# Kernel tuning notes

Measured on AMD Instinct MI355X. Metric: run time of the kernel, lower is better.

Reference implementation:

```python
import jax, jax.numpy as jnp
import numpy as np

GAMMA = 0.01
INFER_STEP = 5


def softor(x, axis, gamma=GAMMA):
    # gamma * logsumexp(x / gamma) along `axis`, rescaled by global max if it exceeds 1
    y = gamma * jax.nn.logsumexp(x / gamma, axis=axis)
    mx = jnp.max(y)
    return jnp.where(mx > 1.0, y / mx, y)


def setup_inputs() -> dict:
    key = jax.random.key(0)
    k1, k2, k3 = jax.random.split(key, 3)
    B, G, C, S, L, m = 32, 2048, 16, 8, 3, 16
    x = jax.random.uniform(k1, (B, G), dtype=jnp.float32)          # valuation vector in [0,1]
    W = jax.random.normal(k2, (m, C), dtype=jnp.float32)           # clause-assignment weights
    I = jax.random.randint(k3, (C, G, S, L), 0, G)                 # index tensor into atom axis
    return {"x": x, "W": W, "I": I}


def reference(x, W, I):
    # x: [B,G] valuations; W: [m,C]; I: [C,G,S,L] int indices into G
    def r(V):
        # all C clause functions at once: gather V along atom axis using I
        gathered = V[:, I]                      # [B,C,G,S,L]
        body = jnp.prod(gathered, axis=-1)      # conjunction over body literals -> [B,C,G,S]
        Cv = softor(body, axis=-1)              # softor over substitutions -> [B,C,G]
        Ws = jax.nn.softmax(W, axis=1)          # [m,C]
        H = jnp.einsum('mc,bcg->mbg', Ws, Cv)   # weighted clause mix -> [m,B,G]
        return softor(H, axis=0)                # softor over m heads -> [B,G]

    R = x
    for _ in range(INFER_STEP):
        R = softor(jnp.stack([R, r(R)], axis=1), axis=1)  # amalgamate old and new facts
    return R
```

## Files before the change

kernel.cpp:

```cpp
#include <hip/hip_runtime.h>

#define GAMMA 0.01f
#define B 32
#define G 2048
#define C 16
#define S 8
#define L 3
#define M 16
#define NBLK 256
#define NTHR 256
#define SLOT_STRIDE 16

#define K_EXP 144.26950408889634f
#define K_LOG 0.006931471805599453f

#define SCOPE __HIP_MEMORY_SCOPE_AGENT

__device__ __forceinline__ void ast(unsigned* p, unsigned v) {
    __hip_atomic_store(p, v, __ATOMIC_RELAXED, SCOPE);
}
__device__ __forceinline__ float aldf(const float* p) {
    return __hip_atomic_load(p, __ATOMIC_RELAXED, SCOPE);
}
__device__ __forceinline__ void astf(float* p, float v) {
    __hip_atomic_store(p, v, __ATOMIC_RELAXED, SCOPE);
}

__device__ __forceinline__ float waveMax(float v) {
#pragma unroll
    for (int off = 32; off > 0; off >>= 1)
        v = fmaxf(v, __shfl_xor(v, off, 64));
    return v;
}

__device__ __forceinline__ float blockMaxBcast(float v, float* scratch) {
    float wm = waveMax(v);
    __syncthreads();
    if ((threadIdx.x & 63) == 0) scratch[threadIdx.x >> 6] = wm;
    __syncthreads();
    return fmaxf(fmaxf(scratch[0], scratch[1]), fmaxf(scratch[2], scratch[3]));
}

__device__ __forceinline__ float gridMaxBarrier(unsigned long long* slot,
                                                unsigned ep, float v,
                                                float* scratch) {
    float wm = waveMax(v);
    __syncthreads();
    if ((threadIdx.x & 63) == 0) scratch[threadIdx.x >> 6] = wm;
    __syncthreads();
    if (threadIdx.x == 0) {
        float bm = fmaxf(fmaxf(scratch[0], scratch[1]),
                         fmaxf(scratch[2], scratch[3]));
        unsigned long long pkt = ((unsigned long long)ep << 32) |
                                 (unsigned long long)__float_as_uint(bm);
        asm volatile("s_waitcnt vmcnt(0) lgkmcnt(0)" ::: "memory");
        __hip_atomic_store(&slot[(size_t)blockIdx.x * SLOT_STRIDE], pkt,
                           __ATOMIC_RELAXED, SCOPE);
    }
    unsigned long long got;
    int guard = 0;
    do {
        got = __hip_atomic_load(&slot[(size_t)threadIdx.x * SLOT_STRIDE],
                                __ATOMIC_RELAXED, SCOPE);
    } while ((unsigned)(got >> 32) < ep && ++guard < (1 << 17));
    return blockMaxBcast(__uint_as_float((unsigned)got), scratch);
}

extern "C" __global__ __launch_bounds__(256) void kmain(
    const float* __restrict__ x, const float* __restrict__ W,
    const int* __restrict__ I,
    unsigned long long* __restrict__ slotA, unsigned long long* __restrict__ slotB,
    unsigned long long* __restrict__ slotC, unsigned* __restrict__ Ipk,
    float* __restrict__ Ry, float* __restrict__ out)
{
    __shared__ __align__(16) float Vrow[G];
    __shared__ float WsL[C * M];
    __shared__ float scratch[4];

    const int t = threadIdx.x;
    const int bid = blockIdx.x;
    const int b = bid & 31;
    const int gt = bid >> 5;
    const int g = (gt << 8) + t;
    const int i = b * G + g;

    {
        const int m = t >> 4, c = t & 15;
        float rmax = -INFINITY;
#pragma unroll
        for (int j = 0; j < C; j++) rmax = fmaxf(rmax, W[m * C + j]);
        float rsum = 0.f;
#pragma unroll
        for (int j = 0; j < C; j++) rsum += __expf(W[m * C + j] - rmax);
        WsL[c * M + m] = __expf(W[m * C + c] - rmax) / rsum;
    }
    {
        const int tid = bid * NTHR + t;
        if (tid < C * G) {
            const int4* ip4 = (const int4*)(I + (size_t)tid * 24);
            int idx[24];
#pragma unroll
            for (int j = 0; j < 6; j++) {
                int4 v = ip4[j];
                idx[4 * j + 0] = v.x; idx[4 * j + 1] = v.y;
                idx[4 * j + 2] = v.z; idx[4 * j + 3] = v.w;
            }
            unsigned* dst = Ipk + (size_t)tid * 12;
#pragma unroll
            for (int j = 0; j < 12; j++)
                ast(&dst[j],
                    ((unsigned)idx[2 * j] << 2) | ((unsigned)idx[2 * j + 1] << 18));
        }
    }
    float m3 = gridMaxBarrier(slotC, 1, -INFINITY, scratch);

    float ry = 0.f;
    for (int it = 0; it < 5; it++) {
        float s = 1.0f;
        if (it > 0)
            s = (m3 > 1.0f) ? 1.0f / m3 : 1.0f;
        if (it == 0) {
            const float4* V4 = (const float4*)(x + (size_t)b * G);
            float4* Vr4 = (float4*)Vrow;
#pragma unroll
            for (int j = 0; j < 2; j++) Vr4[t + j * 256] = V4[t + j * 256];
        } else {
            const float* src = Ry + (size_t)b * G;
#pragma unroll
            for (int j = 0; j < 8; j++) {
                const int gg = t + j * 256;
                Vrow[gg] = s * aldf(&src[gg]);
            }
        }
        __syncthreads();

        float h[M];
#pragma unroll
        for (int m = 0; m < M; m++) h[m] = 0.f;
        float ymax = -INFINITY;
        const char* vb = (const char*)Vrow;

#pragma unroll 4
        for (int c = 0; c < C; c++) {
            const uint4* ip = (const uint4*)(Ipk + ((size_t)c * G + g) * 12);
            uint4 u0 = ip[0], u1 = ip[1], u2 = ip[2];
            unsigned w[12] = {u0.x, u0.y, u0.z, u0.w, u1.x, u1.y,
                              u1.z, u1.w, u2.x, u2.y, u2.z, u2.w};
            float vv[24];
#pragma unroll
            for (int q = 0; q < 12; q++) {
                vv[2 * q]     = *(const float*)(vb + (w[q] & 0xffffu));
                vv[2 * q + 1] = *(const float*)(vb + (w[q] >> 16));
            }
            float body[S];
#pragma unroll
            for (int ss = 0; ss < S; ss++)
                body[ss] = vv[ss * 3] * vv[ss * 3 + 1] * vv[ss * 3 + 2];
            float bm = body[0];
#pragma unroll
            for (int ss = 1; ss < S; ss++) bm = fmaxf(bm, body[ss]);
            float sum = 0.f;
#pragma unroll
            for (int ss = 0; ss < S; ss++)
                sum += exp2f((body[ss] - bm) * K_EXP);
            float y = fmaf(K_LOG, log2f(sum), bm);
            ymax = fmaxf(ymax, y);
#pragma unroll
            for (int m = 0; m < M; m++)
                h[m] = fmaf(WsL[c * M + m], y, h[m]);
        }
        float m1 = gridMaxBarrier(slotA, it + 1, ymax, scratch);

        float hy;
        {
            float s1 = (m1 > 1.0f) ? 1.0f / m1 : 1.0f;
            float hv[M];
            float hm = -INFINITY;
#pragma unroll
            for (int m = 0; m < M; m++) {
                hv[m] = s1 * h[m];
                hm = fmaxf(hm, hv[m]);
            }
            float sum = 0.f;
#pragma unroll
            for (int m = 0; m < M; m++) sum += exp2f((hv[m] - hm) * K_EXP);
            hy = fmaf(K_LOG, log2f(sum), hm);
        }
        float m2 = gridMaxBarrier(slotB, it + 1, hy, scratch);

        {
            float s2 = (m2 > 1.0f) ? 1.0f / m2 : 1.0f;
            float Rv = Vrow[g];
            float rv = s2 * hy;
            float a = fmaxf(Rv, rv), d = fminf(Rv, rv);
            ry = fmaf(K_LOG, log2f(1.0f + exp2f((d - a) * K_EXP)), a);
            astf(&Ry[i], ry);
        }
        m3 = gridMaxBarrier(slotC, it + 2, ry, scratch);
    }

    float sf = (m3 > 1.0f) ? 1.0f / m3 : 1.0f;
    out[i] = sf * ry;
}

extern "C" void kernel_launch(void* const* d_in, const int* in_sizes, int n_in,
                              void* d_out, int out_size, void* d_ws, size_t ws_size,
                              hipStream_t stream) {
    const float* x = (const float*)d_in[0];
    const float* W = (const float*)d_in[1];
    const int*   I = (const int*)d_in[2];
    float* out = (float*)d_out;

    unsigned long long* slotA = (unsigned long long*)d_ws;
    unsigned long long* slotB = slotA + NBLK * SLOT_STRIDE;
    unsigned long long* slotC = slotB + NBLK * SLOT_STRIDE;
    float* Ry = (float*)(slotC + NBLK * SLOT_STRIDE);
    unsigned* Ipk = (unsigned*)(Ry + (size_t)B * G);

    hipMemsetAsync(slotA, 0, 3 * NBLK * SLOT_STRIDE * sizeof(unsigned long long),
                   stream);

    kmain<<<dim3(NBLK), dim3(NTHR), 0, stream>>>(
        x, W, I, slotA, slotB, slotC, Ipk, Ry, out);
}
```

Baseline: 166.6 us.

## Split clause loop across two thread halves with 512-thread blocks

Doubles the block size so each atom is processed by two threads, each handling half of the 16 clauses, and combines the per-head partial sums through a padded shared-memory buffer. The goal is more wavefronts per CU to hide the latency of the gather and transcendental work inside the persistent grid-barrier kernel. The cost is a much larger shared-memory footprint, an extra shared-memory reduction step, and half the threads sitting idle during the head softor and amalgamation phases. The barrier's memory wait now runs on all threads before the block reduction.

After: 160.4 us. 1.04x faster.

```diff
diff --git a/kernel.cpp b/kernel.cpp
--- a/kernel.cpp
+++ b/kernel.cpp
@@ -8,7 +8,7 @@
 #define L 3
 #define M 16
 #define NBLK 256
-#define NTHR 256
+#define NTHR 512
 #define SLOT_STRIDE 16
 
 #define K_EXP 144.26950408889634f
@@ -33,40 +33,41 @@
     return v;
 }
 
-__device__ __forceinline__ float blockMaxBcast(float v, float* scratch) {
-    float wm = waveMax(v);
-    __syncthreads();
-    if ((threadIdx.x & 63) == 0) scratch[threadIdx.x >> 6] = wm;
-    __syncthreads();
-    return fmaxf(fmaxf(scratch[0], scratch[1]), fmaxf(scratch[2], scratch[3]));
+__device__ __forceinline__ float red8(const float* s) {
+    return fmaxf(fmaxf(fmaxf(s[0], s[1]), fmaxf(s[2], s[3])),
+                 fmaxf(fmaxf(s[4], s[5]), fmaxf(s[6], s[7])));
 }
 
 __device__ __forceinline__ float gridMaxBarrier(unsigned long long* slot,
                                                 unsigned ep, float v,
                                                 float* scratch) {
+    asm volatile("s_waitcnt vmcnt(0) lgkmcnt(0)" ::: "memory");
     float wm = waveMax(v);
     __syncthreads();
     if ((threadIdx.x & 63) == 0) scratch[threadIdx.x >> 6] = wm;
     __syncthreads();
     if (threadIdx.x == 0) {
-        float bm = fmaxf(fmaxf(scratch[0], scratch[1]),
-                         fmaxf(scratch[2], scratch[3]));
+        float bm = red8(scratch);
         unsigned long long pkt = ((unsigned long long)ep << 32) |
                                  (unsigned long long)__float_as_uint(bm);
-        asm volatile("s_waitcnt vmcnt(0) lgkmcnt(0)" ::: "memory");
         __hip_atomic_store(&slot[(size_t)blockIdx.x * SLOT_STRIDE], pkt,
                            __ATOMIC_RELAXED, SCOPE);
     }
     unsigned long long got;
     int guard = 0;
     do {
-        got = __hip_atomic_load(&slot[(size_t)threadIdx.x * SLOT_STRIDE],
-                                __ATOMIC_RELAXED, SCOPE);
+        got = __hip_atomic_load(
+            &slot[(size_t)(threadIdx.x & 255) * SLOT_STRIDE],
+            __ATOMIC_RELAXED, SCOPE);
     } while ((unsigned)(got >> 32) < ep && ++guard < (1 << 17));
-    return blockMaxBcast(__uint_as_float((unsigned)got), scratch);
-}
-
-extern "C" __global__ __launch_bounds__(256) void kmain(
+    float pv = waveMax(__uint_as_float((unsigned)got));
+    __syncthreads();
+    if ((threadIdx.x & 63) == 0) scratch[threadIdx.x >> 6] = pv;
+    __syncthreads();
+    return red8(scratch);
+}
+
+extern "C" __global__ __launch_bounds__(512, 2) void kmain(
     const float* __restrict__ x, const float* __restrict__ W,
     const int* __restrict__ I,
     unsigned long long* __restrict__ slotA, unsigned long long* __restrict__ slotB,
@@ -75,16 +76,18 @@
 {
     __shared__ __align__(16) float Vrow[G];
     __shared__ float WsL[C * M];
-    __shared__ float scratch[4];
+    __shared__ float ph[256 * 33];
+    __shared__ float scratch[8];
 
     const int t = threadIdx.x;
     const int bid = blockIdx.x;
     const int b = bid & 31;
     const int gt = bid >> 5;
-    const int g = (gt << 8) + t;
-    const int i = b * G + g;
-
-    {
+    const int ch = t >> 8;
+    const int gl = t & 255;
+    const int g = (gt << 8) + gl;
+
+    if (t < 256) {
         const int m = t >> 4, c = t & 15;
         float rmax = -INFINITY;
 #pragma unroll
@@ -121,14 +124,12 @@
             s = (m3 > 1.0f) ? 1.0f / m3 : 1.0f;
         if (it == 0) {
             const float4* V4 = (const float4*)(x + (size_t)b * G);
-            float4* Vr4 = (float4*)Vrow;
-#pragma unroll
-            for (int j = 0; j < 2; j++) Vr4[t + j * 256] = V4[t + j * 256];
+            ((float4*)Vrow)[t] = V4[t];
         } else {
             const float* src = Ry + (size_t)b * G;
 #pragma unroll
-            for (int j = 0; j < 8; j++) {
-                const int gg = t + j * 256;
+            for (int j = 0; j < 4; j++) {
+                const int gg = t + j * 512;
                 Vrow[gg] = s * aldf(&src[gg]);
             }
         }
@@ -140,8 +141,9 @@
         float ymax = -INFINITY;
         const char* vb = (const char*)Vrow;
 
-#pragma unroll 4
-        for (int c = 0; c < C; c++) {
+#pragma unroll 2
+        for (int cc = 0; cc < 8; cc++) {
+            const int c = ch * 8 + cc;
             const uint4* ip = (const uint4*)(Ipk + ((size_t)c * G + g) * 12);
             uint4 u0 = ip[0], u1 = ip[1], u2 = ip[2];
             unsigned w[12] = {u0.x, u0.y, u0.z, u0.w, u1.x, u1.y,
@@ -169,16 +171,20 @@
             for (int m = 0; m < M; m++)
                 h[m] = fmaf(WsL[c * M + m], y, h[m]);
         }
+#pragma unroll
+        for (int m = 0; m < M; m++)
+            ph[gl * 33 + ch * 16 + m] = h[m];
         float m1 = gridMaxBarrier(slotA, it + 1, ymax, scratch);
 
-        float hy;
-        {
+        float hy = -INFINITY;
+        if (t < 256) {
             float s1 = (m1 > 1.0f) ? 1.0f / m1 : 1.0f;
             float hv[M];
             float hm = -INFINITY;
 #pragma unroll
             for (int m = 0; m < M; m++) {
-                hv[m] = s1 * h[m];
+                float hh = ph[t * 33 + m] + ph[t * 33 + 16 + m];
+                hv[m] = s1 * hh;
                 hm = fmaxf(hm, hv[m]);
             }
             float sum = 0.f;
@@ -188,19 +194,23 @@
         }
         float m2 = gridMaxBarrier(slotB, it + 1, hy, scratch);
 
-        {
+        float rt = -INFINITY;
+        if (t < 256) {
             float s2 = (m2 > 1.0f) ? 1.0f / m2 : 1.0f;
-            float Rv = Vrow[g];
+            float Rv = Vrow[(gt << 8) + t];
             float rv = s2 * hy;
             float a = fmaxf(Rv, rv), d = fminf(Rv, rv);
             ry = fmaf(K_LOG, log2f(1.0f + exp2f((d - a) * K_EXP)), a);
-            astf(&Ry[i], ry);
-        }
-        m3 = gridMaxBarrier(slotC, it + 2, ry, scratch);
-    }
-
-    float sf = (m3 > 1.0f) ? 1.0f / m3 : 1.0f;
-    out[i] = sf * ry;
+            astf(&Ry[(size_t)b * G + (gt << 8) + t], ry);
+            rt = ry;
+        }
+        m3 = gridMaxBarrier(slotC, it + 2, rt, scratch);
+    }
+
+    if (t < 256) {
+        float sf = (m3 > 1.0f) ? 1.0f / m3 : 1.0f;
+        out[(size_t)b * G + (gt << 8) + t] = sf * ry;
+    }
 }
 
 extern "C" void kernel_launch(void* const* d_in, const int* in_sizes, int n_in,
```
